# Kernel optimization log

Hardware: AMD Instinct MI355X
Metric: run time of the kernel (lower is better)

The kernel has to match this reference:

```python
import jax, jax.numpy as jnp
import numpy as np

N, D, NUM_CLASSES = 8192, 1024, 128
ALPHA = 0.1
EPS = 1e-7


def setup_inputs() -> dict:
    key = jax.random.key(0)
    k1, k2 = jax.random.split(key)
    H = jax.random.normal(k1, (N, D), dtype=jnp.float32)
    labels = jax.random.randint(k2, (N,), 0, NUM_CLASSES, dtype=jnp.int64)
    return {"H": H, "labels": labels}


def reference(H, labels):
    n = H.shape[0]
    # squared-euclidean pairwise distances: ||x_i - x_j||^2
    x_norm = jnp.sum(H * H, axis=1)                      # [N]
    dists = x_norm[:, None] + x_norm[None, :] - 2.0 * (H @ H.T)
    dists = jnp.where(jnp.isnan(dists), 0.0, dists)      # dist[dist != dist] = 0
    dists = jnp.maximum(dists, 0.0)                      # clamp(0, inf)
    dists = jnp.maximum(dists, EPS)                      # clamp(min=1e-7)

    diffs = labels[None, :] - labels[:, None]            # [N, N]
    eye = jnp.eye(n, dtype=bool)
    mask_pos = (diffs == 0) & ~eye                       # same label, not self
    mask_neg = diffs != 0                                # different label

    # hardest positive: argmax over positive-masked distances
    anchor_positive_dist = jnp.where(mask_pos, dists, 0.0)
    hardest_positive_idx = jnp.argmax(anchor_positive_dist, axis=1)

    # hard negative: add row-max to non-negatives, take 2nd-smallest (k=1 partition)
    max_neg = jnp.max(dists, axis=1, keepdims=True)
    anchor_negative_dist = dists + max_neg * (1.0 - mask_neg.astype(dists.dtype))
    _, idx2 = jax.lax.top_k(-anchor_negative_dist, 2)    # two smallest per row
    hardest_negatives_idx = idx2[:, 1]

    rows = jnp.arange(n)
    hardest_positive_dist = dists[rows, hardest_positive_idx]
    hardest_negative_dist = dists[rows, hardest_negatives_idx]
    differences = hardest_positive_dist - hardest_negative_dist

    triplet_loss = jnp.maximum(differences + ALPHA, 0.0)  # final='plus', do_max=True
    relevant = triplet_loss > EPS                          # boolean mask (no grad)
    count = jnp.sum(relevant.astype(triplet_loss.dtype))
    return jnp.sum(jnp.where(relevant, triplet_loss, 0.0)) / count
```

## Files before the change

### kernel.cpp

```cpp
#include <hip/hip_runtime.h>
#include <hip/hip_bf16.h>
#include <stdint.h>

constexpr int Nn = 8192;
constexpr int Dd = 1024;
constexpr float kAlpha = 0.1f;
constexpr float kEps = 1e-7f;
constexpr float kInf = 3.0e38f;

constexpr int BM = 128, BN = 128, BK = 32;
constexpr int NB = Nn / BM;
constexpr int NPAIR = NB * (NB + 1) / 2;

using bfx8 = __attribute__((ext_vector_type(8))) __bf16;
using f32x4 = __attribute__((ext_vector_type(4))) float;

__device__ __forceinline__ unsigned short f2bf(float f) {
  union { float f; unsigned int u; } v; v.f = f;
  unsigned int u = v.u;
  u = u + 0x7fffu + ((u >> 16) & 1u);
  return (unsigned short)(u >> 16);
}

__device__ __forceinline__ void min2_insert(float& m1, float& m2, float x) {
  const float lo = fminf(m1, x);
  const float hi = fmaxf(m1, x);
  m1 = lo;
  m2 = fminf(m2, hi);
}

__device__ __forceinline__ void min2_merge(float& m1, float& m2, float o1, float o2) {
  m2 = fminf(fminf(m2, o2), fmaxf(m1, o1));
  m1 = fminf(m1, o1);
}

__global__ __launch_bounds__(256) void prep_kernel(const float* __restrict__ H,
                                                   unsigned short* __restrict__ Hb,
                                                   float* __restrict__ xn) {
  const int wave = threadIdx.x >> 6;
  const int lane = threadIdx.x & 63;
  const int row = blockIdx.x * 4 + wave;
  const float4* src = (const float4*)(H + (size_t)row * Dd);
  ushort4* dst = (ushort4*)(Hb + (size_t)row * Dd);
  float acc = 0.f;
#pragma unroll
  for (int i = 0; i < 4; ++i) {
    float4 v = src[lane + 64 * i];
    acc = fmaf(v.x, v.x, acc);
    acc = fmaf(v.y, v.y, acc);
    acc = fmaf(v.z, v.z, acc);
    acc = fmaf(v.w, v.w, acc);
    ushort4 o;
    o.x = f2bf(v.x); o.y = f2bf(v.y); o.z = f2bf(v.z); o.w = f2bf(v.w);
    dst[lane + 64 * i] = o;
  }
#pragma unroll
  for (int off = 32; off; off >>= 1) acc += __shfl_xor(acc, off, 64);
  if (lane == 0) xn[row] = acc;
}

__global__ __launch_bounds__(256, 4) void triplet_main(
    const unsigned short* __restrict__ Hb, const float* __restrict__ xn,
    const int* __restrict__ lab, float* __restrict__ wsMax,
    float* __restrict__ wsM1, float* __restrict__ wsM2) {
  __shared__ __align__(16) unsigned char smem[32768];

  const int tid = threadIdx.x;
  const int wave = tid >> 6;
  const int lane = tid & 63;
  const int quad = lane >> 4;
  const int l15 = lane & 15;
  const int wm = wave & 1;
  const int wn = wave >> 1;

  int b = blockIdx.x, I = 0;
  while (b >= NB - I) { b -= NB - I; ++I; }
  const int J = I + b;
  const bool diag = (I == J);

  const int rowBase = I * BM;
  const int colBase = J * BN;

  int lr[16]; float xr[16];
#pragma unroll
  for (int m = 0; m < 4; ++m)
#pragma unroll
    for (int r = 0; r < 4; ++r) {
      const int row = rowBase + wm * 64 + m * 16 + quad * 4 + r;
      lr[m * 4 + r] = lab[row];
      xr[m * 4 + r] = xn[row];
    }
  int lc[4]; float xc[4];
#pragma unroll
  for (int n = 0; n < 4; ++n) {
    const int col = colBase + wn * 64 + n * 16 + l15;
    lc[n] = lab[col];
    xc[n] = xn[col];
  }

  const int stRow = wave * 32 + (lane >> 2);
  const int stCol = (lane & 3) * 8;
  const unsigned short* gA = Hb + (size_t)(rowBase + stRow) * Dd + stCol;
  const unsigned short* gB = Hb + (size_t)(colBase + stRow) * Dd + stCol;

  auto stage = [&](int buf, int kt) {
    unsigned short* s = (unsigned short*)(smem + (buf << 14));
#pragma unroll
    for (int j = 0; j < 2; ++j) {
      __builtin_amdgcn_global_load_lds(
          (const __attribute__((address_space(1))) void*)(gA + j * 16 * Dd + kt),
          (__attribute__((address_space(3))) void*)&s[(wave * 2 + j) * 512],
          16, 0, 0);
      __builtin_amdgcn_global_load_lds(
          (const __attribute__((address_space(1))) void*)(gB + j * 16 * Dd + kt),
          (__attribute__((address_space(3))) void*)&s[4096 + (wave * 2 + j) * 512],
          16, 0, 0);
    }
  };

  f32x4 acc[4][4];
#pragma unroll
  for (int m = 0; m < 4; ++m)
#pragma unroll
    for (int n = 0; n < 4; ++n) acc[m][n] = {0.f, 0.f, 0.f, 0.f};

  stage(0, 0);
  __syncthreads();

  constexpr int KIT = Dd / BK;
  for (int it = 0; it < KIT; ++it) {
    const int cur = it & 1;
    if (it + 1 < KIT) stage(cur ^ 1, (it + 1) * BK);

    const unsigned short* s = (const unsigned short*)(smem + (cur << 14));
    bfx8 a[4], bb[4];
#pragma unroll
    for (int m = 0; m < 4; ++m)
      a[m] = *(const bfx8*)&s[(wm * 64 + m * 16 + l15) * BK + quad * 8];
#pragma unroll
    for (int n = 0; n < 4; ++n)
      bb[n] = *(const bfx8*)&s[4096 + (wn * 64 + n * 16 + l15) * BK + quad * 8];
#pragma unroll
    for (int m = 0; m < 4; ++m)
#pragma unroll
      for (int n = 0; n < 4; ++n)
        acc[m][n] = __builtin_amdgcn_mfma_f32_16x16x32_bf16(a[m], bb[n], acc[m][n], 0, 0, 0);

    __syncthreads();
  }

  float maxp[16], mn1[16], mn2[16];
#pragma unroll
  for (int s = 0; s < 16; ++s) { maxp[s] = 0.f; mn1[s] = kInf; mn2[s] = kInf; }
  float tmaxp[4], tmn1[4], tmn2[4];
#pragma unroll
  for (int n = 0; n < 4; ++n) { tmaxp[n] = 0.f; tmn1[n] = kInf; tmn2[n] = kInf; }

  if (!diag) {
#pragma unroll
    for (int m = 0; m < 4; ++m)
#pragma unroll
      for (int n = 0; n < 4; ++n)
#pragma unroll
        for (int r = 0; r < 4; ++r) {
          const int s = m * 4 + r;
          const float d = fmaf(-2.f, acc[m][n][r], xr[s] + xc[n]);
          const bool eq = (lr[s] == lc[n]);
          const float pos = eq ? d : 0.f;
          const float dn = eq ? kInf : d;
          maxp[s] = fmaxf(maxp[s], pos);
          min2_insert(mn1[s], mn2[s], dn);
          tmaxp[n] = fmaxf(tmaxp[n], pos);
          min2_insert(tmn1[n], tmn2[n], dn);
        }
  } else {
#pragma unroll
    for (int m = 0; m < 4; ++m)
#pragma unroll
      for (int n = 0; n < 4; ++n)
#pragma unroll
        for (int r = 0; r < 4; ++r) {
          const int s = m * 4 + r;
          const bool selfp = (wm == wn) && (m == n) && (quad * 4 + r == l15);
          const float d = fmaf(-2.f, acc[m][n][r], xr[s] + xc[n]);
          const bool eq = (lr[s] == lc[n]);
          const float pos = (eq && !selfp) ? d : 0.f;
          const float dn = eq ? kInf : d;
          maxp[s] = fmaxf(maxp[s], pos);
          min2_insert(mn1[s], mn2[s], dn);
        }
  }

#pragma unroll
  for (int off = 1; off < 16; off <<= 1) {
#pragma unroll
    for (int s = 0; s < 16; ++s) {
      const float om = __shfl_xor(maxp[s], off, 64);
      const float o1 = __shfl_xor(mn1[s], off, 64);
      const float o2 = __shfl_xor(mn2[s], off, 64);
      maxp[s] = fmaxf(maxp[s], om);
      min2_merge(mn1[s], mn2[s], o1, o2);
    }
  }

  float* rbuf = (float*)smem;
  float* tbm = ((float*)smem) + 384;
  float* tb1 = tbm + 1024;
  float* tb2 = tb1 + 1024;

  if (wn == 1 && l15 == 0) {
#pragma unroll
    for (int m = 0; m < 4; ++m)
#pragma unroll
      for (int r = 0; r < 4; ++r) {
        const int s = m * 4 + r;
        const int local = m * 16 + quad * 4 + r;
        rbuf[(wm * 64 + local) * 3 + 0] = maxp[s];
        rbuf[(wm * 64 + local) * 3 + 1] = mn1[s];
        rbuf[(wm * 64 + local) * 3 + 2] = mn2[s];
      }
  }
#pragma unroll
  for (int n = 0; n < 4; ++n) {
    const int idx = (((wm * 2 + wn) * 4 + quad) * 4 + n) * 16 + l15;
    tbm[idx] = tmaxp[n];
    tb1[idx] = tmn1[n];
    tb2[idx] = tmn2[n];
  }
  __syncthreads();

  if (wn == 0 && l15 == 0) {
#pragma unroll
    for (int m = 0; m < 4; ++m)
#pragma unroll
      for (int r = 0; r < 4; ++r) {
        const int s = m * 4 + r;
        const int local = m * 16 + quad * 4 + r;
        float om = rbuf[(wm * 64 + local) * 3 + 0];
        float o1 = rbuf[(wm * 64 + local) * 3 + 1];
        float o2 = rbuf[(wm * 64 + local) * 3 + 2];
        const float M = fmaxf(maxp[s], om);
        float a1 = mn1[s], a2 = mn2[s];
        min2_merge(a1, a2, o1, o2);
        const size_t p = ((size_t)(I * NB + J)) * 128 + wm * 64 + local;
        wsMax[p] = M;
        wsM1[p] = a1;
        wsM2[p] = a2;
      }
  }
  if (wm == 0 && !diag) {
    const int tn = lane >> 4;
    const int tl = lane & 15;
    float M = 0.f, a1 = kInf, a2 = kInf;
#pragma unroll
    for (int wm2 = 0; wm2 < 2; ++wm2)
#pragma unroll
      for (int q = 0; q < 4; ++q) {
        const int idx = (((wm2 * 2 + wn) * 4 + q) * 4 + tn) * 16 + tl;
        M = fmaxf(M, tbm[idx]);
        min2_merge(a1, a2, tb1[idx], tb2[idx]);
      }
    const size_t p = ((size_t)(J * NB + I)) * 128 + wn * 64 + lane;
    wsMax[p] = M;
    wsM1[p] = a1;
    wsM2[p] = a2;
  }
}

__global__ __launch_bounds__(256) void merge_kernel(
    const float* __restrict__ wsMax, const float* __restrict__ wsM1,
    const float* __restrict__ wsM2, float* __restrict__ bsum,
    float* __restrict__ bcnt) {
  const int rl = threadIdx.x & 31;
  const int p = threadIdx.x >> 5;
  const int row = blockIdx.x * 32 + rl;
  const int bi = row >> 7;
  const int rr = row & 127;
  float mp = 0.f, m1 = kInf, m2 = kInf;
#pragma unroll
  for (int k = 0; k < 8; ++k) {
    const int bj = p * 8 + k;
    const size_t idx = ((size_t)(bi * NB + bj)) * 128 + rr;
    mp = fmaxf(mp, wsMax[idx]);
    min2_merge(m1, m2, wsM1[idx], wsM2[idx]);
  }
  __shared__ float sm[8][32], s1[8][32], s2[8][32];
  sm[p][rl] = mp; s1[p][rl] = m1; s2[p][rl] = m2;
  __syncthreads();
  float ls = 0.f, lc = 0.f;
  if (threadIdx.x < 32) {
    mp = sm[0][rl]; m1 = s1[0][rl]; m2 = s2[0][rl];
#pragma unroll
    for (int q = 1; q < 8; ++q) {
      mp = fmaxf(mp, sm[q][rl]);
      min2_merge(m1, m2, s1[q][rl], s2[q][rl]);
    }
    const float loss = fmaxf(mp - m2 + kAlpha, 0.f);
    ls = (loss > kEps) ? loss : 0.f;
    lc = (loss > kEps) ? 1.f : 0.f;
  }
  if (threadIdx.x < 64) {
#pragma unroll
    for (int off = 32; off; off >>= 1) {
      ls += __shfl_down(ls, off, 64);
      lc += __shfl_down(lc, off, 64);
    }
    if (threadIdx.x == 0) { bsum[blockIdx.x] = ls; bcnt[blockIdx.x] = lc; }
  }
}

__global__ __launch_bounds__(256) void final_kernel(const float* __restrict__ bsum,
                                                    const float* __restrict__ bcnt,
                                                    float* __restrict__ out) {
  float s = bsum[threadIdx.x];
  float c = bcnt[threadIdx.x];
#pragma unroll
  for (int off = 32; off; off >>= 1) {
    s += __shfl_down(s, off, 64);
    c += __shfl_down(c, off, 64);
  }
  __shared__ float ss[4], sc[4];
  const int w = threadIdx.x >> 6;
  if ((threadIdx.x & 63) == 0) { ss[w] = s; sc[w] = c; }
  __syncthreads();
  if (threadIdx.x == 0)
    out[0] = (ss[0] + ss[1] + ss[2] + ss[3]) / (sc[0] + sc[1] + sc[2] + sc[3]);
}

extern "C" void kernel_launch(void* const* d_in, const int* in_sizes, int n_in,
                              void* d_out, int out_size, void* d_ws, size_t ws_size,
                              hipStream_t stream) {
  (void)in_sizes; (void)n_in; (void)out_size; (void)ws_size;
  const float* H = (const float*)d_in[0];
  const int* lab = (const int*)d_in[1];
  float* out = (float*)d_out;

  char* ws = (char*)d_ws;
  unsigned short* Hb = (unsigned short*)ws;
  float* xn = (float*)(ws + (size_t)Nn * Dd * sizeof(unsigned short));
  float* wsMax = xn + Nn;
  float* wsM1 = wsMax + NB * NB * 128;
  float* wsM2 = wsM1 + NB * NB * 128;
  float* bsum = wsM2 + NB * NB * 128;
  float* bcnt = bsum + 256;

  prep_kernel<<<Nn / 4, 256, 0, stream>>>(H, Hb, xn);
  triplet_main<<<NPAIR, 256, 0, stream>>>(Hb, xn, lab, wsMax, wsM1, wsM2);
  merge_kernel<<<256, 256, 0, stream>>>(wsMax, wsM1, wsM2, bsum, bcnt);
  final_kernel<<<1, 256, 0, stream>>>(bsum, bcnt, out);
}
```

Baseline: 217.8 us.

## Unroll K loop by two with static LDS buffers, relax occupancy, coalesce row stores

The K loop is manually unrolled by two so each half uses a compile-time-constant shared-memory buffer index, removing dynamic buffer addressing. Launch bounds drop from 4 to 2 waves per SIMD minimum, giving the compiler more registers at the cost of possible lower occupancy. The row-partial results are now combined in shared memory in a struct-of-arrays layout and written to global memory by 128 threads in a coalesced way, instead of scattered strided writes from a few lanes. This adds one more block barrier.

```diff
diff --git a/kernel.cpp b/kernel.cpp
--- a/kernel.cpp
+++ b/kernel.cpp
@@ -59,7 +59,7 @@
   if (lane == 0) xn[row] = acc;
 }
 
-__global__ __launch_bounds__(256, 4) void triplet_main(
+__global__ __launch_bounds__(256, 2) void triplet_main(
     const unsigned short* __restrict__ Hb, const float* __restrict__ xn,
     const int* __restrict__ lab, float* __restrict__ wsMax,
     float* __restrict__ wsM1, float* __restrict__ wsM2) {
@@ -124,15 +124,8 @@
 #pragma unroll
     for (int n = 0; n < 4; ++n) acc[m][n] = {0.f, 0.f, 0.f, 0.f};
 
-  stage(0, 0);
-  __syncthreads();
-
-  constexpr int KIT = Dd / BK;
-  for (int it = 0; it < KIT; ++it) {
-    const int cur = it & 1;
-    if (it + 1 < KIT) stage(cur ^ 1, (it + 1) * BK);
-
-    const unsigned short* s = (const unsigned short*)(smem + (cur << 14));
+  auto compute = [&](int buf) {
+    const unsigned short* s = (const unsigned short*)(smem + (buf << 14));
     bfx8 a[4], bb[4];
 #pragma unroll
     for (int m = 0; m < 4; ++m)
@@ -145,7 +138,18 @@
 #pragma unroll
       for (int n = 0; n < 4; ++n)
         acc[m][n] = __builtin_amdgcn_mfma_f32_16x16x32_bf16(a[m], bb[n], acc[m][n], 0, 0, 0);
-
+  };
+
+  stage(0, 0);
+  __syncthreads();
+
+  constexpr int KIT = Dd / BK;
+  for (int k0 = 0; k0 < KIT; k0 += 2) {
+    stage(1, (k0 + 1) * BK);
+    compute(0);
+    __syncthreads();
+    if (k0 + 2 < KIT) stage(0, (k0 + 2) * BK);
+    compute(1);
     __syncthreads();
   }
 
@@ -203,8 +207,11 @@
     }
   }
 
-  float* rbuf = (float*)smem;
-  float* tbm = ((float*)smem) + 384;
+  float* f = (float*)smem;
+  float* rbm = f;
+  float* rb1 = f + 128;
+  float* rb2 = f + 256;
+  float* tbm = f + 384;
   float* tb1 = tbm + 1024;
   float* tb2 = tb1 + 1024;
 
@@ -214,10 +221,10 @@
 #pragma unroll
       for (int r = 0; r < 4; ++r) {
         const int s = m * 4 + r;
-        const int local = m * 16 + quad * 4 + r;
-        rbuf[(wm * 64 + local) * 3 + 0] = maxp[s];
-        rbuf[(wm * 64 + local) * 3 + 1] = mn1[s];
-        rbuf[(wm * 64 + local) * 3 + 2] = mn2[s];
+        const int local = wm * 64 + m * 16 + quad * 4 + r;
+        rbm[local] = maxp[s];
+        rb1[local] = mn1[s];
+        rb2[local] = mn2[s];
       }
   }
 #pragma unroll
@@ -235,17 +242,12 @@
 #pragma unroll
       for (int r = 0; r < 4; ++r) {
         const int s = m * 4 + r;
-        const int local = m * 16 + quad * 4 + r;
-        float om = rbuf[(wm * 64 + local) * 3 + 0];
-        float o1 = rbuf[(wm * 64 + local) * 3 + 1];
-        float o2 = rbuf[(wm * 64 + local) * 3 + 2];
-        const float M = fmaxf(maxp[s], om);
+        const int local = wm * 64 + m * 16 + quad * 4 + r;
+        rbm[local] = fmaxf(maxp[s], rbm[local]);
         float a1 = mn1[s], a2 = mn2[s];
-        min2_merge(a1, a2, o1, o2);
-        const size_t p = ((size_t)(I * NB + J)) * 128 + wm * 64 + local;
-        wsMax[p] = M;
-        wsM1[p] = a1;
-        wsM2[p] = a2;
+        min2_merge(a1, a2, rb1[local], rb2[local]);
+        rb1[local] = a1;
+        rb2[local] = a2;
       }
   }
   if (wm == 0 && !diag) {
@@ -264,6 +266,13 @@
     wsMax[p] = M;
     wsM1[p] = a1;
     wsM2[p] = a2;
+  }
+  __syncthreads();
+  if (tid < 128) {
+    const size_t p = ((size_t)(I * NB + J)) * 128 + tid;
+    wsMax[p] = rbm[tid];
+    wsM1[p] = rb1[tid];
+    wsM2[p] = rb2[tid];
   }
 }
 
```

Result: faster. 202.0 us (-7.2%).
